# Kernel tuning notes

Hardware: AMD Instinct MI355X
Metric: run time of the kernel (lower is better)

## Reference

```python
import jax, jax.numpy as jnp
import numpy as np
import math

DIM = 2048
N_PHASES = 8
B, L = 4, 4096


def setup_inputs() -> dict:
    key = jax.random.key(0)
    ks = jax.random.split(key, 12)
    s = 0.02
    return {
        "x": jax.random.normal(ks[0], (B, L, DIM), dtype=jnp.float32),
        # weights stored [in, out] (transposed vs torch Linear)
        "Wp": jax.random.normal(ks[1], (DIM, N_PHASES), dtype=jnp.float32) * s,
        "bp": jnp.zeros((N_PHASES,), dtype=jnp.float32),
        "Wa": jax.random.normal(ks[2], (DIM, N_PHASES), dtype=jnp.float32) * s,
        "ba": jnp.zeros((N_PHASES,), dtype=jnp.float32),
        "Wv": jax.random.normal(ks[3], (DIM, DIM), dtype=jnp.float32) * s,
        "bv": jnp.zeros((DIM,), dtype=jnp.float32),
        "ln_g": jnp.ones((DIM,), dtype=jnp.float32),
        "ln_b": jnp.zeros((DIM,), dtype=jnp.float32),
        "Wo": jax.random.normal(ks[4], (DIM, DIM), dtype=jnp.float32) * s,
        "bo": jnp.zeros((DIM,), dtype=jnp.float32),
    }


def _layernorm(h, g, b, eps=1e-5):
    mu = jnp.mean(h, axis=-1, keepdims=True)
    var = jnp.var(h, axis=-1, keepdims=True)
    return (h - mu) * jax.lax.rsqrt(var + eps) * g + b


def reference(x, Wp, bp, Wa, ba, Wv, bv, ln_g, ln_b, Wo, bo):
    Llen = x.shape[1]
    phase = jnp.tanh(x @ Wp + bp) * math.pi          # [B,L,P]
    amp = jax.nn.softplus(x @ Wa + ba) + 0.1         # [B,L,P]
    value = x @ Wv + bv                              # [B,L,D]
    # (value[...,None,:] * cos_p[...,None] * amp[...,None]).sum(-2)
    # == value * sum_p(cos_p * amp)  -- algebraic factorization, same math.
    cr = jnp.sum(jnp.cos(phase) * amp, axis=-1, keepdims=True)  # [B,L,1]
    ci = jnp.sum(jnp.sin(phase) * amp, axis=-1, keepdims=True)  # [B,L,1]
    bound = value * (cr + ci)                        # real+imag combined
    retrieved = jnp.cumsum(bound, axis=1)            # [B,L,D]
    h = _layernorm(retrieved / math.sqrt(Llen), ln_g, ln_b)
    return x + h @ Wo + bo
```

## Files before the change

### kernel.cpp

```cpp
#include <hip/hip_runtime.h>

#define DIM   2048
#define LSEQ  4096
#define BATCH 4
#define NTOK  (BATCH*LSEQ)
#define NCH   16
#define CHL   (LSEQ/NCH)
#define PI_F  3.14159265358979f
#define NT    (DIM/64)

typedef __bf16 bf16x8 __attribute__((ext_vector_type(8)));
typedef float  f32x4  __attribute__((ext_vector_type(4)));
typedef float  f32x8  __attribute__((ext_vector_type(8)));
typedef unsigned short ushort4_t __attribute__((ext_vector_type(4)));
typedef unsigned short ushort8 __attribute__((ext_vector_type(8)));

__device__ __forceinline__ unsigned short f2bf(float f) {
    unsigned int u = __float_as_uint(f);
    u += 0x7fffu + ((u >> 16) & 1u);
    return (unsigned short)(u >> 16);
}
__device__ __forceinline__ float bf2f(unsigned short u) {
    return __uint_as_float((unsigned int)u << 16);
}

__device__ __forceinline__ void gload_lds16(const void* g, void* l) {
    __builtin_amdgcn_global_load_lds(
        (const __attribute__((address_space(1))) void*)g,
        (__attribute__((address_space(3))) void*)l, 16, 0, 0);
}

__global__ __launch_bounds__(256) void k_transpose(const float* __restrict__ src,
                                                   unsigned short* __restrict__ dst) {
    __shared__ float tile[32][33];
    int tx = threadIdx.x, ty = threadIdx.y;
    int k0 = blockIdx.y * 32, n0 = blockIdx.x * 32;
#pragma unroll
    for (int r = 0; r < 4; r++)
        tile[ty + r * 8][tx] = src[(size_t)(k0 + ty + r * 8) * DIM + n0 + tx];
    __syncthreads();
#pragma unroll
    for (int r = 0; r < 4; r++)
        dst[(size_t)(n0 + ty + r * 8) * DIM + k0 + tx] = f2bf(tile[tx][ty + r * 8]);
}

__global__ __launch_bounds__(256) void k_prep_wpa(const float* __restrict__ Wp,
                                                  const float* __restrict__ Wa,
                                                  unsigned short* __restrict__ WpaT) {
    int idx = blockIdx.x * 256 + threadIdx.x;
    int p = idx >> 11, k = idx & (DIM - 1);
    float v = (p < 8) ? Wp[(size_t)k * 8 + p] : Wa[(size_t)k * 8 + (p - 8)];
    WpaT[idx] = f2bf(v);
}

__global__ __launch_bounds__(256) void k_sproj_mfma(const float* __restrict__ x,
                                                    const unsigned short* __restrict__ WpaT,
                                                    const float* __restrict__ bp,
                                                    const float* __restrict__ ba,
                                                    float* __restrict__ s,
                                                    unsigned short* __restrict__ xbf) {
    const int t = threadIdx.x;
    const int w = t >> 6, l = t & 63;
    const int r16 = l & 15, q = l >> 4;
    const int rowbase = blockIdx.x * 64 + w * 16;
    const float* xr = x + (size_t)(rowbase + r16) * DIM + q * 8;
    unsigned short* xw = xbf + (size_t)(rowbase + r16) * DIM + q * 8;
    const unsigned short* wrow = WpaT + r16 * DIM + q * 8;

    f32x4 acc = {};
#pragma unroll 8
    for (int ks = 0; ks < 64; ks++) {
        f32x8 xv = *(const f32x8*)(xr + ks * 32);
        ushort8 xo;
#pragma unroll
        for (int j = 0; j < 8; j++) xo[j] = f2bf(xv[j]);
        *(ushort8*)(xw + ks * 32) = xo;
        bf16x8 av = *(const bf16x8*)&xo;
        bf16x8 bv = *(const bf16x8*)(wrow + ks * 32);
        acc = __builtin_amdgcn_mfma_f32_16x16x32_bf16(av, bv, acc, 0, 0, 0);
    }
    const float bpv = bp[r16 & 7], bav = ba[r16 & 7];
#pragma unroll
    for (int j = 0; j < 4; j++) {
        float z = acc[j];
        float zo = __shfl_xor(z, 8);
        float zp = z + bpv, za = zo + bav;
        float ph = tanhf(zp) * PI_F;
        float amp = (za > 20.f ? za : log1pf(expf(za))) + 0.1f;
        float term = (r16 < 8) ? (cosf(ph) + sinf(ph)) * amp : 0.f;
        term += __shfl_xor(term, 1);
        term += __shfl_xor(term, 2);
        term += __shfl_xor(term, 4);
        if (r16 == 0) s[rowbase + q * 4 + j] = term;
    }
}

__device__ __forceinline__ void stage_unit(const unsigned short* __restrict__ src,
                                           unsigned short* dst, int tid) {
    gload_lds16(src,                     dst + tid * 8);
    gload_lds16(src + (size_t)128 * DIM, dst + (tid + 512) * 8);
}

template <int EPI>
__global__ __launch_bounds__(512, 2) void k_gemm256(const unsigned short* __restrict__ A,
                                                    const unsigned short* __restrict__ Bt,
                                                    const float* __restrict__ bias,
                                                    const float* __restrict__ sc,
                                                    const unsigned short* __restrict__ residbf,
                                                    float* __restrict__ C,
                                                    unsigned short* __restrict__ Cbf,
                                                    float* __restrict__ part) {
    __shared__ __align__(16) unsigned short As[2][2][256 * 32];
    __shared__ __align__(16) unsigned short Bs[2][2][256 * 32];
    __shared__ float colsum[2][256];
    const int tid = threadIdx.x;
    const int w = tid >> 6, lane = tid & 63;
    const int wm = w >> 2, wn = w & 3;
    const int r16 = lane & 15, q = lane >> 4;

    int bid = blockIdx.x;
    int wgs = (bid & 7) * 64 + (bid >> 3);
    int tm = wgs >> 3, tn = wgs & 7;
    int brow = tm * 256, bcol = tn * 256;

    const int kq = ((tid & 3) ^ ((tid >> 3) & 3)) * 8;
    const unsigned short* pA = A  + (size_t)(brow + (tid >> 2)) * DIM + kq;
    const unsigned short* pB = Bt + (size_t)(bcol + (tid >> 2)) * DIM + kq;

    const int qs8 = (q ^ ((r16 >> 1) & 3)) * 8;
    const int offA = (wm * 128 + r16) * 32 + qs8;
    const int offB = (wn * 64  + r16) * 32 + qs8;

    f32x4 acc[8][4] = {};

    stage_unit(pA,      &As[0][0][0], tid);
    stage_unit(pB,      &Bs[0][0][0], tid);
    stage_unit(pA + 32, &As[0][1][0], tid);
    stage_unit(pB + 32, &Bs[0][1][0], tid);
    stage_unit(pA + 64, &As[1][0][0], tid);
    asm volatile("s_waitcnt vmcnt(6)" ::: "memory");
    __builtin_amdgcn_s_barrier();

    for (int t = 0; t < NT; ++t) {
        const int s = t & 1;
        unsigned short* A0 = &As[s][0][0];
        unsigned short* A1 = &As[s][1][0];
        unsigned short* B0 = &Bs[s][0][0];
        unsigned short* B1 = &Bs[s][1][0];
        unsigned short* nA1 = &As[s ^ 1][1][0];
        unsigned short* nB0 = &Bs[s ^ 1][0][0];
        unsigned short* nB1 = &Bs[s ^ 1][1][0];
        const unsigned short* pAn = pA + (t + 1) * 64;
        const unsigned short* pBn = pB + (t + 1) * 64;

        bf16x8 aF[4], bF[4];
#pragma unroll
        for (int i = 0; i < 4; i++) aF[i] = *(const bf16x8*)(A0 + offA + i * 512);
#pragma unroll
        for (int i = 0; i < 4; i++) bF[i] = *(const bf16x8*)(B0 + offB + i * 512);
        stage_unit(pBn, nB0, tid);
        __builtin_amdgcn_s_barrier();
        __builtin_amdgcn_s_setprio(1);
#pragma unroll
        for (int i = 0; i < 4; i++)
#pragma unroll
            for (int n = 0; n < 4; n++)
                acc[i][n] = __builtin_amdgcn_mfma_f32_16x16x32_bf16(aF[i], bF[n], acc[i][n], 0, 0, 0);
        __builtin_amdgcn_s_setprio(0);
        __builtin_amdgcn_s_barrier();

#pragma unroll
        for (int i = 0; i < 4; i++) aF[i] = *(const bf16x8*)(A0 + offA + 2048 + i * 512);
        stage_unit(pAn + 32, nA1, tid);
        __builtin_amdgcn_s_barrier();
        __builtin_amdgcn_s_setprio(1);
#pragma unroll
        for (int i = 0; i < 4; i++)
#pragma unroll
            for (int n = 0; n < 4; n++)
                acc[4 + i][n] = __builtin_amdgcn_mfma_f32_16x16x32_bf16(aF[i], bF[n], acc[4 + i][n], 0, 0, 0);
        __builtin_amdgcn_s_setprio(0);
        asm volatile("s_waitcnt vmcnt(6)" ::: "memory");
        __builtin_amdgcn_s_barrier();

#pragma unroll
        for (int i = 0; i < 4; i++) aF[i] = *(const bf16x8*)(A1 + offA + i * 512);
#pragma unroll
        for (int i = 0; i < 4; i++) bF[i] = *(const bf16x8*)(B1 + offB + i * 512);
        stage_unit(pBn + 32, nB1, tid);
        __builtin_amdgcn_s_barrier();
        __builtin_amdgcn_s_setprio(1);
#pragma unroll
        for (int i = 0; i < 4; i++)
#pragma unroll
            for (int n = 0; n < 4; n++)
                acc[i][n] = __builtin_amdgcn_mfma_f32_16x16x32_bf16(aF[i], bF[n], acc[i][n], 0, 0, 0);
        __builtin_amdgcn_s_setprio(0);
        __builtin_amdgcn_s_barrier();

#pragma unroll
        for (int i = 0; i < 4; i++) aF[i] = *(const bf16x8*)(A1 + offA + 2048 + i * 512);
        stage_unit(pA + (t + 2) * 64, A0, tid);
        __builtin_amdgcn_s_barrier();
        __builtin_amdgcn_s_setprio(1);
#pragma unroll
        for (int i = 0; i < 4; i++)
#pragma unroll
            for (int n = 0; n < 4; n++)
                acc[4 + i][n] = __builtin_amdgcn_mfma_f32_16x16x32_bf16(aF[i], bF[n], acc[4 + i][n], 0, 0, 0);
        __builtin_amdgcn_s_setprio(0);
        asm volatile("s_waitcnt vmcnt(6)" ::: "memory");
        __builtin_amdgcn_s_barrier();
    }
    asm volatile("s_waitcnt vmcnt(0)" ::: "memory");

    float cs[4] = {0.f, 0.f, 0.f, 0.f};
#pragma unroll
    for (int mf = 0; mf < 8; mf++) {
        int r0 = brow + wm * 128 + mf * 16 + q * 4;
#pragma unroll
        for (int nf = 0; nf < 4; nf++) {
            int c = bcol + wn * 64 + nf * 16 + r16;
            float bc = bias[c];
#pragma unroll
            for (int j = 0; j < 4; j++) {
                int r = r0 + j;
                float v = acc[mf][nf][j] + bc;
                if (EPI == 0) {
                    v *= sc[r];
                    cs[nf] += v;
                    Cbf[(size_t)r * DIM + c] = f2bf(v);
                } else {
                    v += bf2f(residbf[(size_t)r * DIM + c]);
                    C[(size_t)r * DIM + c] = v;
                }
            }
        }
    }
    if (EPI == 0) {
#pragma unroll
        for (int nf = 0; nf < 4; nf++) {
            float v = cs[nf];
            v += __shfl_xor(v, 16);
            v += __shfl_xor(v, 32);
            if (q == 0) colsum[wm][wn * 64 + nf * 16 + r16] = v;
        }
        __syncthreads();
        if (tid < 256)
            part[(size_t)(brow >> 8) * DIM + bcol + tid] = colsum[0][tid] + colsum[1][tid];
    }
}

__global__ __launch_bounds__(256) void k_scan_offsets(float* __restrict__ part) {
    int tid = blockIdx.x * 256 + threadIdx.x;
    int d = tid & (DIM - 1);
    int b = tid >> 11;
    float run = 0.f;
    for (int ch = 0; ch < NCH; ch++) {
        size_t idx = ((size_t)b * NCH + ch) * DIM + d;
        float v = part[idx];
        part[idx] = run;
        run += v;
    }
}

__global__ __launch_bounds__(256) void k_scan_apply(unsigned short* __restrict__ boundbf,
                                                    const float* __restrict__ part) {
    int tid = blockIdx.x * 256 + threadIdx.x;
    int d = tid & (DIM - 1);
    int ch = (tid >> 11) & (NCH - 1);
    int b = tid >> 15;
    float run = part[tid];
    unsigned short* p = boundbf + ((size_t)b * LSEQ + (size_t)ch * CHL) * DIM + d;
    for (int i = 0; i < CHL; i++) {
        run += bf2f(p[(size_t)i * DIM]);
        p[(size_t)i * DIM] = f2bf(run);
    }
}

__global__ __launch_bounds__(256) void k_lnorm(const unsigned short* __restrict__ retbf,
                                               const float* __restrict__ g,
                                               const float* __restrict__ bta,
                                               unsigned short* __restrict__ h) {
    int row = blockIdx.x, t = threadIdx.x;
    ushort8 rv = *(const ushort8*)(retbf + (size_t)row * DIM + t * 8);
    const float scl = 1.0f / 64.0f;
    float vv[8];
    float sum = 0.f, ss = 0.f;
#pragma unroll
    for (int j = 0; j < 8; j++) {
        vv[j] = bf2f(rv[j]) * scl;
        sum += vv[j];
        ss  += vv[j] * vv[j];
    }
#pragma unroll
    for (int off = 32; off; off >>= 1) { sum += __shfl_down(sum, off); ss += __shfl_down(ss, off); }
    __shared__ float red[4][2];
    __shared__ float mu_s, rstd_s;
    int w = t >> 6, lane = t & 63;
    if (lane == 0) { red[w][0] = sum; red[w][1] = ss; }
    __syncthreads();
    if (t == 0) {
        float S = red[0][0] + red[1][0] + red[2][0] + red[3][0];
        float Q = red[0][1] + red[1][1] + red[2][1] + red[3][1];
        float mu = S / DIM;
        float var = Q / DIM - mu * mu;
        mu_s = mu; rstd_s = rsqrtf(var + 1e-5f);
    }
    __syncthreads();
    float mu = mu_s, rstd = rstd_s;
    f32x8 gv = *(const f32x8*)(g + t * 8);
    f32x8 bv = *(const f32x8*)(bta + t * 8);
    ushort8 o;
#pragma unroll
    for (int j = 0; j < 8; j++) o[j] = f2bf((vv[j] - mu) * rstd * gv[j] + bv[j]);
    *(ushort8*)(h + (size_t)row * DIM + t * 8) = o;
}

extern "C" void kernel_launch(void* const* d_in, const int* in_sizes, int n_in,
                              void* d_out, int out_size, void* d_ws, size_t ws_size,
                              hipStream_t stream) {
    const float* x   = (const float*)d_in[0];
    const float* Wp  = (const float*)d_in[1];
    const float* bp  = (const float*)d_in[2];
    const float* Wa  = (const float*)d_in[3];
    const float* ba  = (const float*)d_in[4];
    const float* Wv  = (const float*)d_in[5];
    const float* bv  = (const float*)d_in[6];
    const float* lng = (const float*)d_in[7];
    const float* lnb = (const float*)d_in[8];
    const float* Wo  = (const float*)d_in[9];
    const float* bo  = (const float*)d_in[10];
    float* out = (float*)d_out;

    char* ws = (char*)d_ws;
    unsigned short* x_bf  = (unsigned short*)ws; ws += (size_t)NTOK * DIM * 2;
    unsigned short* h_bf  = (unsigned short*)ws; ws += (size_t)NTOK * DIM * 2;
    unsigned short* WvT   = (unsigned short*)ws; ws += (size_t)DIM * DIM * 2;
    unsigned short* WoT   = (unsigned short*)ws; ws += (size_t)DIM * DIM * 2;
    unsigned short* WpaT  = (unsigned short*)ws; ws += (size_t)16 * DIM * 2;
    float* svec           = (float*)ws;          ws += (size_t)NTOK * 4;
    unsigned short* bound = (unsigned short*)ws; ws += (size_t)NTOK * DIM * 2;
    float* part           = (float*)ws;          ws += (size_t)BATCH * NCH * DIM * 4;

    dim3 tb(32, 8);
    k_transpose<<<dim3(64, 64), tb, 0, stream>>>(Wv, WvT);
    k_transpose<<<dim3(64, 64), tb, 0, stream>>>(Wo, WoT);
    k_prep_wpa<<<128, 256, 0, stream>>>(Wp, Wa, WpaT);
    k_sproj_mfma<<<NTOK / 64, 256, 0, stream>>>(x, WpaT, bp, ba, svec, x_bf);

    k_gemm256<0><<<512, 512, 0, stream>>>(x_bf, WvT, bv, svec, nullptr, nullptr, bound, part);

    k_scan_offsets<<<BATCH * DIM / 256, 256, 0, stream>>>(part);
    k_scan_apply<<<BATCH * NCH * DIM / 256, 256, 0, stream>>>(bound, part);

    k_lnorm<<<NTOK, 256, 0, stream>>>(bound, lng, lnb, h_bf);

    k_gemm256<1><<<512, 512, 0, stream>>>(h_bf, WoT, bo, nullptr, x_bf, out, nullptr, nullptr);
}
```

Before: 401.4 us.

## Shrink GEMM tiles to 128x128 with 256 threads and finer scan chunks

Replaces the 256x256-tile, 512-thread GEMM with a 128x128-tile, 256-thread version that has four times as many blocks. The K-loop pipeline drops from four barrier phases to two per iteration. The partial column sums and scan chunking change from 16 to 32 chunks of 128 rows to match the new tile height. The aim is better occupancy and load balance across CUs and shorter serial scan chains. In exchange, operand reuse per tile falls, so more global and LDS traffic is spent per MFMA.

```diff
diff --git a/kernel.cpp b/kernel.cpp
--- a/kernel.cpp
+++ b/kernel.cpp
@@ -4,15 +4,14 @@
 #define LSEQ  4096
 #define BATCH 4
 #define NTOK  (BATCH*LSEQ)
-#define NCH   16
-#define CHL   (LSEQ/NCH)
+#define NCH2  32
+#define CHL2  128
 #define PI_F  3.14159265358979f
 #define NT    (DIM/64)
 
 typedef __bf16 bf16x8 __attribute__((ext_vector_type(8)));
 typedef float  f32x4  __attribute__((ext_vector_type(4)));
 typedef float  f32x8  __attribute__((ext_vector_type(8)));
-typedef unsigned short ushort4_t __attribute__((ext_vector_type(4)));
 typedef unsigned short ushort8 __attribute__((ext_vector_type(8)));
 
 __device__ __forceinline__ unsigned short f2bf(float f) {
@@ -97,12 +96,12 @@
 
 __device__ __forceinline__ void stage_unit(const unsigned short* __restrict__ src,
                                            unsigned short* dst, int tid) {
-    gload_lds16(src,                     dst + tid * 8);
-    gload_lds16(src + (size_t)128 * DIM, dst + (tid + 512) * 8);
+    gload_lds16(src,                    dst + tid * 8);
+    gload_lds16(src + (size_t)64 * DIM, dst + (tid + 256) * 8);
 }
 
 template <int EPI>
-__global__ __launch_bounds__(512, 2) void k_gemm256(const unsigned short* __restrict__ A,
+__global__ __launch_bounds__(256, 2) void k_gemm128(const unsigned short* __restrict__ A,
                                                     const unsigned short* __restrict__ Bt,
                                                     const float* __restrict__ bias,
                                                     const float* __restrict__ sc,
@@ -110,28 +109,28 @@
                                                     float* __restrict__ C,
                                                     unsigned short* __restrict__ Cbf,
                                                     float* __restrict__ part) {
-    __shared__ __align__(16) unsigned short As[2][2][256 * 32];
-    __shared__ __align__(16) unsigned short Bs[2][2][256 * 32];
-    __shared__ float colsum[2][256];
+    __shared__ __align__(16) unsigned short As[2][2][128 * 32];
+    __shared__ __align__(16) unsigned short Bs[2][2][128 * 32];
+    __shared__ float colsum[2][128];
     const int tid = threadIdx.x;
     const int w = tid >> 6, lane = tid & 63;
-    const int wm = w >> 2, wn = w & 3;
+    const int wm = w >> 1, wn = w & 1;
     const int r16 = lane & 15, q = lane >> 4;
 
     int bid = blockIdx.x;
-    int wgs = (bid & 7) * 64 + (bid >> 3);
-    int tm = wgs >> 3, tn = wgs & 7;
-    int brow = tm * 256, bcol = tn * 256;
+    int wgs = (bid & 7) * 256 + (bid >> 3);
+    int tm = wgs >> 4, tn = wgs & 15;
+    int brow = tm * 128, bcol = tn * 128;
 
     const int kq = ((tid & 3) ^ ((tid >> 3) & 3)) * 8;
     const unsigned short* pA = A  + (size_t)(brow + (tid >> 2)) * DIM + kq;
     const unsigned short* pB = Bt + (size_t)(bcol + (tid >> 2)) * DIM + kq;
 
     const int qs8 = (q ^ ((r16 >> 1) & 3)) * 8;
-    const int offA = (wm * 128 + r16) * 32 + qs8;
-    const int offB = (wn * 64  + r16) * 32 + qs8;
-
-    f32x4 acc[8][4] = {};
+    const int offA = (wm * 64 + r16) * 32 + qs8;
+    const int offB = (wn * 64 + r16) * 32 + qs8;
+
+    f32x4 acc[4][4] = {};
 
     stage_unit(pA,      &As[0][0][0], tid);
     stage_unit(pB,      &Bs[0][0][0], tid);
@@ -141,25 +140,17 @@
     asm volatile("s_waitcnt vmcnt(6)" ::: "memory");
     __builtin_amdgcn_s_barrier();
 
+#pragma unroll 2
     for (int t = 0; t < NT; ++t) {
         const int s = t & 1;
-        unsigned short* A0 = &As[s][0][0];
-        unsigned short* A1 = &As[s][1][0];
-        unsigned short* B0 = &Bs[s][0][0];
-        unsigned short* B1 = &Bs[s][1][0];
-        unsigned short* nA1 = &As[s ^ 1][1][0];
-        unsigned short* nB0 = &Bs[s ^ 1][0][0];
-        unsigned short* nB1 = &Bs[s ^ 1][1][0];
-        const unsigned short* pAn = pA + (t + 1) * 64;
-        const unsigned short* pBn = pB + (t + 1) * 64;
-
         bf16x8 aF[4], bF[4];
-#pragma unroll
-        for (int i = 0; i < 4; i++) aF[i] = *(const bf16x8*)(A0 + offA + i * 512);
-#pragma unroll
-        for (int i = 0; i < 4; i++) bF[i] = *(const bf16x8*)(B0 + offB + i * 512);
-        stage_unit(pBn, nB0, tid);
-        __builtin_amdgcn_s_barrier();
+
+#pragma unroll
+        for (int i = 0; i < 4; i++) aF[i] = *(const bf16x8*)(&As[s][0][0] + offA + i * 512);
+#pragma unroll
+        for (int n = 0; n < 4; n++) bF[n] = *(const bf16x8*)(&Bs[s][0][0] + offB + n * 512);
+        stage_unit(pB + (t + 1) * 64,      &Bs[s ^ 1][0][0], tid);
+        stage_unit(pA + (t + 1) * 64 + 32, &As[s ^ 1][1][0], tid);
         __builtin_amdgcn_s_setprio(1);
 #pragma unroll
         for (int i = 0; i < 4; i++)
@@ -167,28 +158,15 @@
             for (int n = 0; n < 4; n++)
                 acc[i][n] = __builtin_amdgcn_mfma_f32_16x16x32_bf16(aF[i], bF[n], acc[i][n], 0, 0, 0);
         __builtin_amdgcn_s_setprio(0);
+        asm volatile("s_waitcnt vmcnt(4)" ::: "memory");
         __builtin_amdgcn_s_barrier();
 
 #pragma unroll
-        for (int i = 0; i < 4; i++) aF[i] = *(const bf16x8*)(A0 + offA + 2048 + i * 512);
-        stage_unit(pAn + 32, nA1, tid);
-        __builtin_amdgcn_s_barrier();
-        __builtin_amdgcn_s_setprio(1);
-#pragma unroll
-        for (int i = 0; i < 4; i++)
-#pragma unroll
-            for (int n = 0; n < 4; n++)
-                acc[4 + i][n] = __builtin_amdgcn_mfma_f32_16x16x32_bf16(aF[i], bF[n], acc[4 + i][n], 0, 0, 0);
-        __builtin_amdgcn_s_setprio(0);
-        asm volatile("s_waitcnt vmcnt(6)" ::: "memory");
-        __builtin_amdgcn_s_barrier();
-
-#pragma unroll
-        for (int i = 0; i < 4; i++) aF[i] = *(const bf16x8*)(A1 + offA + i * 512);
-#pragma unroll
-        for (int i = 0; i < 4; i++) bF[i] = *(const bf16x8*)(B1 + offB + i * 512);
-        stage_unit(pBn + 32, nB1, tid);
-        __builtin_amdgcn_s_barrier();
+        for (int i = 0; i < 4; i++) aF[i] = *(const bf16x8*)(&As[s][1][0] + offA + i * 512);
+#pragma unroll
+        for (int n = 0; n < 4; n++) bF[n] = *(const bf16x8*)(&Bs[s][1][0] + offB + n * 512);
+        stage_unit(pB + (t + 1) * 64 + 32, &Bs[s ^ 1][1][0], tid);
+        stage_unit(pA + (t + 2) * 64,      &As[s][0][0], tid);
         __builtin_amdgcn_s_setprio(1);
 #pragma unroll
         for (int i = 0; i < 4; i++)
@@ -196,28 +174,15 @@
             for (int n = 0; n < 4; n++)
                 acc[i][n] = __builtin_amdgcn_mfma_f32_16x16x32_bf16(aF[i], bF[n], acc[i][n], 0, 0, 0);
         __builtin_amdgcn_s_setprio(0);
+        asm volatile("s_waitcnt vmcnt(4)" ::: "memory");
         __builtin_amdgcn_s_barrier();
-
-#pragma unroll
-        for (int i = 0; i < 4; i++) aF[i] = *(const bf16x8*)(A1 + offA + 2048 + i * 512);
-        stage_unit(pA + (t + 2) * 64, A0, tid);
-        __builtin_amdgcn_s_barrier();
-        __builtin_amdgcn_s_setprio(1);
-#pragma unroll
-        for (int i = 0; i < 4; i++)
-#pragma unroll
-            for (int n = 0; n < 4; n++)
-                acc[4 + i][n] = __builtin_amdgcn_mfma_f32_16x16x32_bf16(aF[i], bF[n], acc[4 + i][n], 0, 0, 0);
-        __builtin_amdgcn_s_setprio(0);
-        asm volatile("s_waitcnt vmcnt(6)" ::: "memory");
-        __builtin_amdgcn_s_barrier();
     }
     asm volatile("s_waitcnt vmcnt(0)" ::: "memory");
 
     float cs[4] = {0.f, 0.f, 0.f, 0.f};
 #pragma unroll
-    for (int mf = 0; mf < 8; mf++) {
-        int r0 = brow + wm * 128 + mf * 16 + q * 4;
+    for (int mf = 0; mf < 4; mf++) {
+        int r0 = brow + wm * 64 + mf * 16 + q * 4;
 #pragma unroll
         for (int nf = 0; nf < 4; nf++) {
             int c = bcol + wn * 64 + nf * 16 + r16;
@@ -246,8 +211,8 @@
             if (q == 0) colsum[wm][wn * 64 + nf * 16 + r16] = v;
         }
         __syncthreads();
-        if (tid < 256)
-            part[(size_t)(brow >> 8) * DIM + bcol + tid] = colsum[0][tid] + colsum[1][tid];
+        if (tid < 128)
+            part[(size_t)(brow >> 7) * DIM + bcol + tid] = colsum[0][tid] + colsum[1][tid];
     }
 }
 
@@ -256,8 +221,8 @@
     int d = tid & (DIM - 1);
     int b = tid >> 11;
     float run = 0.f;
-    for (int ch = 0; ch < NCH; ch++) {
-        size_t idx = ((size_t)b * NCH + ch) * DIM + d;
+    for (int ch = 0; ch < NCH2; ch++) {
+        size_t idx = ((size_t)b * NCH2 + ch) * DIM + d;
         float v = part[idx];
         part[idx] = run;
         run += v;
@@ -268,11 +233,11 @@
                                                     const float* __restrict__ part) {
     int tid = blockIdx.x * 256 + threadIdx.x;
     int d = tid & (DIM - 1);
-    int ch = (tid >> 11) & (NCH - 1);
-    int b = tid >> 15;
+    int ch = (tid >> 11) & (NCH2 - 1);
+    int b = tid >> 16;
     float run = part[tid];
-    unsigned short* p = boundbf + ((size_t)b * LSEQ + (size_t)ch * CHL) * DIM + d;
-    for (int i = 0; i < CHL; i++) {
+    unsigned short* p = boundbf + ((size_t)b * LSEQ + (size_t)ch * CHL2) * DIM + d;
+    for (int i = 0; i < CHL2; i++) {
         run += bf2f(p[(size_t)i * DIM]);
         p[(size_t)i * DIM] = f2bf(run);
     }
@@ -341,7 +306,7 @@
     unsigned short* WpaT  = (unsigned short*)ws; ws += (size_t)16 * DIM * 2;
     float* svec           = (float*)ws;          ws += (size_t)NTOK * 4;
     unsigned short* bound = (unsigned short*)ws; ws += (size_t)NTOK * DIM * 2;
-    float* part           = (float*)ws;          ws += (size_t)BATCH * NCH * DIM * 4;
+    float* part           = (float*)ws;          ws += (size_t)BATCH * NCH2 * DIM * 4;
 
     dim3 tb(32, 8);
     k_transpose<<<dim3(64, 64), tb, 0, stream>>>(Wv, WvT);
@@ -349,12 +314,12 @@
     k_prep_wpa<<<128, 256, 0, stream>>>(Wp, Wa, WpaT);
     k_sproj_mfma<<<NTOK / 64, 256, 0, stream>>>(x, WpaT, bp, ba, svec, x_bf);
 
-    k_gemm256<0><<<512, 512, 0, stream>>>(x_bf, WvT, bv, svec, nullptr, nullptr, bound, part);
+    k_gemm128<0><<<2048, 256, 0, stream>>>(x_bf, WvT, bv, svec, nullptr, nullptr, bound, part);
 
     k_scan_offsets<<<BATCH * DIM / 256, 256, 0, stream>>>(part);
-    k_scan_apply<<<BATCH * NCH * DIM / 256, 256, 0, stream>>>(bound, part);
+    k_scan_apply<<<BATCH * NCH2 * DIM / 256, 256, 0, stream>>>(bound, part);
 
     k_lnorm<<<NTOK, 256, 0, stream>>>(bound, lng, lnb, h_bf);
 
-    k_gemm256<1><<<512, 512, 0, stream>>>(h_bf, WoT, bo, nullptr, x_bf, out, nullptr, nullptr);
-}
+    k_gemm128<1><<<2048, 256, 0, stream>>>(h_bf, WoT, bo, nullptr, x_bf, out, nullptr, nullptr);
+}
```

After: 479.5 us. 1.19x slower.

## Double-buffer MFMA register fragments to overlap LDS reads with matrix math

Applied to the files above, without the earlier changes.

Restructures the GEMM main loop so that LDS fragment loads for the next sub-step go into a second set of registers while the MFMAs for the current sub-step run. This removes one barrier per phase and changes the vmcnt waits from 6 to 4. The aim is to hide LDS read latency behind MFMA issue. In exchange it raises VGPR pressure from the extra fragment registers and the unroll-by-2, which could lower occupancy or cause spills, and the changed wait counts and barrier placement risk LDS read/write races.

```diff
diff --git a/kernel.cpp b/kernel.cpp
--- a/kernel.cpp
+++ b/kernel.cpp
@@ -12,7 +12,6 @@
 typedef __bf16 bf16x8 __attribute__((ext_vector_type(8)));
 typedef float  f32x4  __attribute__((ext_vector_type(4)));
 typedef float  f32x8  __attribute__((ext_vector_type(8)));
-typedef unsigned short ushort4_t __attribute__((ext_vector_type(4)));
 typedef unsigned short ushort8 __attribute__((ext_vector_type(8)));
 
 __device__ __forceinline__ unsigned short f2bf(float f) {
@@ -132,6 +131,7 @@
     const int offB = (wn * 64  + r16) * 32 + qs8;
 
     f32x4 acc[8][4] = {};
+    bf16x8 aA[4], aB[4], bA[4], bB[4];
 
     stage_unit(pA,      &As[0][0][0], tid);
     stage_unit(pB,      &Bs[0][0][0], tid);
@@ -140,79 +140,77 @@
     stage_unit(pA + 64, &As[1][0][0], tid);
     asm volatile("s_waitcnt vmcnt(6)" ::: "memory");
     __builtin_amdgcn_s_barrier();
-
+#pragma unroll
+    for (int i = 0; i < 4; i++) aA[i] = *(const bf16x8*)(&As[0][0][0] + offA + i * 512);
+#pragma unroll
+    for (int n = 0; n < 4; n++) bA[n] = *(const bf16x8*)(&Bs[0][0][0] + offB + n * 512);
+
+#pragma unroll 2
     for (int t = 0; t < NT; ++t) {
         const int s = t & 1;
         unsigned short* A0 = &As[s][0][0];
         unsigned short* A1 = &As[s][1][0];
-        unsigned short* B0 = &Bs[s][0][0];
         unsigned short* B1 = &Bs[s][1][0];
-        unsigned short* nA1 = &As[s ^ 1][1][0];
+        unsigned short* nA0 = &As[s ^ 1][0][0];
         unsigned short* nB0 = &Bs[s ^ 1][0][0];
-        unsigned short* nB1 = &Bs[s ^ 1][1][0];
-        const unsigned short* pAn = pA + (t + 1) * 64;
-        const unsigned short* pBn = pB + (t + 1) * 64;
-
-        bf16x8 aF[4], bF[4];
-#pragma unroll
-        for (int i = 0; i < 4; i++) aF[i] = *(const bf16x8*)(A0 + offA + i * 512);
-#pragma unroll
-        for (int i = 0; i < 4; i++) bF[i] = *(const bf16x8*)(B0 + offB + i * 512);
-        stage_unit(pBn, nB0, tid);
+
+        stage_unit(pB + (t + 1) * 64, nB0, tid);
+#pragma unroll
+        for (int i = 0; i < 4; i++) aB[i] = *(const bf16x8*)(A0 + offA + 2048 + i * 512);
+        __builtin_amdgcn_s_setprio(1);
+#pragma unroll
+        for (int i = 0; i < 4; i++)
+#pragma unroll
+            for (int n = 0; n < 4; n++)
+                acc[i][n] = __builtin_amdgcn_mfma_f32_16x16x32_bf16(aA[i], bA[n], acc[i][n], 0, 0, 0);
+        __builtin_amdgcn_s_setprio(0);
+        asm volatile("s_waitcnt vmcnt(4)" ::: "memory");
         __builtin_amdgcn_s_barrier();
+
+        stage_unit(pA + (t + 1) * 64 + 32, &As[s ^ 1][1][0], tid);
+#pragma unroll
+        for (int i = 0; i < 4; i++) aA[i] = *(const bf16x8*)(A1 + offA + i * 512);
+#pragma unroll
+        for (int n = 0; n < 4; n++) bB[n] = *(const bf16x8*)(B1 + offB + n * 512);
         __builtin_amdgcn_s_setprio(1);
 #pragma unroll
         for (int i = 0; i < 4; i++)
 #pragma unroll
             for (int n = 0; n < 4; n++)
-                acc[i][n] = __builtin_amdgcn_mfma_f32_16x16x32_bf16(aF[i], bF[n], acc[i][n], 0, 0, 0);
+                acc[4 + i][n] = __builtin_amdgcn_mfma_f32_16x16x32_bf16(aB[i], bA[n], acc[4 + i][n], 0, 0, 0);
         __builtin_amdgcn_s_setprio(0);
+        asm volatile("s_waitcnt vmcnt(4)" ::: "memory");
         __builtin_amdgcn_s_barrier();
 
-#pragma unroll
-        for (int i = 0; i < 4; i++) aF[i] = *(const bf16x8*)(A0 + offA + 2048 + i * 512);
-        stage_unit(pAn + 32, nA1, tid);
+        stage_unit(pB + (t + 1) * 64 + 32, &Bs[s ^ 1][1][0], tid);
+#pragma unroll
+        for (int i = 0; i < 4; i++) aB[i] = *(const bf16x8*)(A1 + offA + 2048 + i * 512);
+        __builtin_amdgcn_s_setprio(1);
+#pragma unroll
+        for (int i = 0; i < 4; i++)
+#pragma unroll
+            for (int n = 0; n < 4; n++)
+                acc[i][n] = __builtin_amdgcn_mfma_f32_16x16x32_bf16(aA[i], bB[n], acc[i][n], 0, 0, 0);
+        __builtin_amdgcn_s_setprio(0);
+        asm volatile("s_waitcnt vmcnt(4)" ::: "memory");
         __builtin_amdgcn_s_barrier();
+
+        stage_unit(pA + (t + 2) * 64, A0, tid);
+#pragma unroll
+        for (int i = 0; i < 4; i++) aA[i] = *(const bf16x8*)(nA0 + offA + i * 512);
+#pragma unroll
+        for (int n = 0; n < 4; n++) bA[n] = *(const bf16x8*)(nB0 + offB + n * 512);
         __builtin_amdgcn_s_setprio(1);
 #pragma unroll
         for (int i = 0; i < 4; i++)
 #pragma unroll
             for (int n = 0; n < 4; n++)
-                acc[4 + i][n] = __builtin_amdgcn_mfma_f32_16x16x32_bf16(aF[i], bF[n], acc[4 + i][n], 0, 0, 0);
+                acc[4 + i][n] = __builtin_amdgcn_mfma_f32_16x16x32_bf16(aB[i], bB[n], acc[4 + i][n], 0, 0, 0);
         __builtin_amdgcn_s_setprio(0);
-        asm volatile("s_waitcnt vmcnt(6)" ::: "memory");
+        asm volatile("s_waitcnt vmcnt(4)" ::: "memory");
         __builtin_amdgcn_s_barrier();
-
-#pragma unroll
-        for (int i = 0; i < 4; i++) aF[i] = *(const bf16x8*)(A1 + offA + i * 512);
-#pragma unroll
-        for (int i = 0; i < 4; i++) bF[i] = *(const bf16x8*)(B1 + offB + i * 512);
-        stage_unit(pBn + 32, nB1, tid);
-        __builtin_amdgcn_s_barrier();
-        __builtin_amdgcn_s_setprio(1);
-#pragma unroll
-        for (int i = 0; i < 4; i++)
-#pragma unroll
-            for (int n = 0; n < 4; n++)
-                acc[i][n] = __builtin_amdgcn_mfma_f32_16x16x32_bf16(aF[i], bF[n], acc[i][n], 0, 0, 0);
-        __builtin_amdgcn_s_setprio(0);
-        __builtin_amdgcn_s_barrier();
-
-#pragma unroll
-        for (int i = 0; i < 4; i++) aF[i] = *(const bf16x8*)(A1 + offA + 2048 + i * 512);
-        stage_unit(pA + (t + 2) * 64, A0, tid);
-        __builtin_amdgcn_s_barrier();
-        __builtin_amdgcn_s_setprio(1);
-#pragma unroll
-        for (int i = 0; i < 4; i++)
-#pragma unroll
-            for (int n = 0; n < 4; n++)
-                acc[4 + i][n] = __builtin_amdgcn_mfma_f32_16x16x32_bf16(aF[i], bF[n], acc[4 + i][n], 0, 0, 0);
-        __builtin_amdgcn_s_setprio(0);
-        asm volatile("s_waitcnt vmcnt(6)" ::: "memory");
-        __builtin_amdgcn_s_barrier();
-    }
-    asm volatile("s_waitcnt vmcnt(0)" ::: "memory");
+    }
+    asm volatile("s_waitcnt vmcnt(0) lgkmcnt(0)" ::: "memory");
 
     float cs[4] = {0.f, 0.f, 0.f, 0.f};
 #pragma unroll
```

Measured after the change: 402.8 us. No clear change (+0.4%).
